# Kernel tuning notes

Hardware: AMD Instinct MI355X
Metric: run time of the kernel (lower is better)

Reference implementation:

```python
import jax, jax.numpy as jnp
import numpy as np

EPS = 1e-5
NUM_HEADS = 8

def _bn(x, w, b, m, v):
    # inference-mode BatchNorm2d over channel dim of (B,C,H,W)
    inv = w / jnp.sqrt(v + EPS)
    return x * inv[None, :, None, None] + (b - m * inv)[None, :, None, None]

def _conv1x1(x, W, b):
    # 1x1 conv == per-pixel matmul: W is (out_ch, in_ch)
    return jnp.einsum('bchw,ec->behw', x, W) + b[None, :, None, None]

def _forward(x, bn1_w, bn1_b, bn1_m, bn1_v, Wq, bq, Wk, bk, Wv, bv, gamma, temperature,
             conv_w, conv_b, cbn_w, cbn_b, cbn_m, cbn_v, rs_w, rs_b, rbn_w, rbn_b, rbn_m, rbn_v):
    B, C, Wd, Hd = x.shape
    S = Wd * Hd
    E = Wq.shape[0]
    hd = E // NUM_HEADS
    xa = jax.nn.relu(_bn(x, bn1_w, bn1_b, bn1_m, bn1_v))
    def proj(Wm, bm):
        return _conv1x1(xa, Wm, bm).reshape(B, NUM_HEADS, hd, S).transpose(0, 1, 3, 2)  # (B,h,S,d)
    q = proj(Wq, bq)
    k = proj(Wk, bk)
    v = proj(Wv, bv)
    scores = jnp.einsum('bhsd,bhtd->bhst', q, k) / temperature  # (B,h,S,S)
    scores = scores - jnp.max(scores, axis=-1, keepdims=True)   # redundant amax-subtract as in source
    attn = jax.nn.softmax(scores, axis=-1)
    out = jnp.einsum('bhst,bhtd->bhsd', attn, v)
    out = out.transpose(0, 1, 3, 2).reshape(B, E, Wd, Hd)
    conv_path = jax.nn.relu(_bn(_conv1x1(x, conv_w, conv_b), cbn_w, cbn_b, cbn_m, cbn_v))
    fused = gamma[0] * out + conv_path
    return jax.nn.gelu(_bn(_conv1x1(fused, rs_w, rs_b), rbn_w, rbn_b, rbn_m, rbn_v), approximate=False)

def setup_inputs() -> dict:
    key = jax.random.key(0)
    ks = jax.random.split(key, 18)
    C, E = 256, 512
    n = lambda k, s, sc=0.02: jax.random.normal(k, s, jnp.float32) * sc
    return {
        'x': jax.random.normal(ks[0], (1, C, 64, 64), jnp.float32),
        'bn1_w': 1.0 + n(ks[1], (C,), 0.1), 'bn1_b': n(ks[2], (C,), 0.1),
        'bn1_m': n(ks[3], (C,), 0.05), 'bn1_v': 0.5 + jax.random.uniform(ks[4], (C,), jnp.float32),
        'Wq': n(ks[5], (E, C)), 'bq': jnp.zeros((E,), jnp.float32),
        'Wk': n(ks[6], (E, C)), 'bk': jnp.zeros((E,), jnp.float32),
        'Wv': n(ks[7], (E, C)), 'bv': jnp.zeros((E,), jnp.float32),
        'gamma': jnp.full((1,), 0.5, jnp.float32),
        'temperature': jnp.asarray(0.85, jnp.float32),
        'conv_w': n(ks[8], (E, C)), 'conv_b': jnp.zeros((E,), jnp.float32),
        'cbn_w': 1.0 + n(ks[9], (E,), 0.1), 'cbn_b': n(ks[10], (E,), 0.1),
        'cbn_m': n(ks[11], (E,), 0.05), 'cbn_v': 0.5 + jax.random.uniform(ks[12], (E,), jnp.float32),
        'rs_w': n(ks[13], (C, E)), 'rs_b': jnp.zeros((C,), jnp.float32),
        'rbn_w': 1.0 + n(ks[14], (C,), 0.1), 'rbn_b': n(ks[15], (C,), 0.1),
        'rbn_m': n(ks[16], (C,), 0.05), 'rbn_v': 0.5 + jax.random.uniform(ks[17], (C,), jnp.float32),
    }

def reference(x, bn1_w, bn1_b, bn1_m, bn1_v, Wq, bq, Wk, bk, Wv, bv, gamma, temperature,
              conv_w, conv_b, cbn_w, cbn_b, cbn_m, cbn_v, rs_w, rs_b, rbn_w, rbn_b, rbn_m, rbn_v):
    return _forward(x, bn1_w, bn1_b, bn1_m, bn1_v, Wq, bq, Wk, bk, Wv, bv, gamma, temperature,
                    conv_w, conv_b, cbn_w, cbn_b, cbn_m, cbn_v, rs_w, rs_b, rbn_w, rbn_b, rbn_m, rbn_v)
```

## Files before the change

kernel.cpp:

```cpp
#include <hip/hip_runtime.h>

#define S_DIM 4096
#define C_IN  256
#define E_DIM 512
#define HD    64
#define EPSV  1e-5f

typedef __attribute__((ext_vector_type(8))) short s8v;
typedef __attribute__((ext_vector_type(4))) short s4v;
typedef __attribute__((ext_vector_type(4))) float f4v;
typedef __attribute__((ext_vector_type(16))) float f16v;

__device__ __forceinline__ float bf2f(unsigned short h){
  union{unsigned u; float f;} v; v.u = ((unsigned)h)<<16; return v.f;
}
__device__ __forceinline__ unsigned short f2bf(float f){
  union{float f; unsigned u;} v; v.f = f;
  unsigned r = v.u + 0x7fffu + ((v.u>>16)&1u);
  return (unsigned short)(r>>16);
}
__device__ __forceinline__ unsigned cvtpk_bf16(float lo, float hi_){
  unsigned r;
  asm("v_cvt_pk_bf16_f32 %0, %1, %2" : "=v"(r) : "v"(lo), "v"(hi_));
  return r;
}
__device__ __forceinline__ s8v lds_rd8(const unsigned short* b, int row, int ck){
  return *(const s8v*)&b[(row<<6) + (((ck)^(row&7))<<3)];
}
__device__ __forceinline__ void lds_wr8(unsigned short* b, int row, int ck, s8v v){
  *(s8v*)&b[(row<<6) + (((ck)^(row&7))<<3)] = v;
}
__device__ __forceinline__ s4v lds_rd4q(const unsigned short* b, int row, int q4){
  return *(const s4v*)&b[(row<<6) + (((q4)^(row&15))<<2)];
}
__device__ __forceinline__ void gl_lds16(const unsigned short* g, unsigned short* l){
  __builtin_amdgcn_global_load_lds(
      (const __attribute__((address_space(1))) unsigned int*)g,
      (__attribute__((address_space(3))) unsigned int*)l, 16, 0, 0);
}

__global__ __launch_bounds__(256) void k_wcvt(const float* __restrict__ w0,
    const float* __restrict__ w1, const float* __restrict__ w2,
    const float* __restrict__ w3, const float* __restrict__ w4,
    unsigned short* __restrict__ dst){
  int i = blockIdx.x*256 + threadIdx.x;
  int z = blockIdx.y;
  const float* s = (z==0)?w0:(z==1)?w1:(z==2)?w2:(z==3)?w3:w4;
  dst[z*(E_DIM*C_IN) + i] = f2bf(s[i]);
}

__global__ __launch_bounds__(256) void k_prep(const float* __restrict__ x,
    const float* __restrict__ bw, const float* __restrict__ bb,
    const float* __restrict__ bm, const float* __restrict__ bvar,
    unsigned short* __restrict__ XaT, unsigned short* __restrict__ XrT){
  __shared__ float tile[32][33];
  int tid = threadIdx.x;
  int tx = tid & 31, ty = tid >> 5;
  int s0 = blockIdx.x*32, c0 = blockIdx.y*32;
  #pragma unroll
  for(int p=0;p<4;p++){
    int c = c0 + ty + p*8;
    tile[ty+p*8][tx] = x[c*S_DIM + s0 + tx];
  }
  __syncthreads();
  int cc = c0 + tx;
  float inv  = bw[cc] * rsqrtf(bvar[cc] + EPSV);
  float beta = bb[cc] - bm[cc]*inv;
  #pragma unroll
  for(int p=0;p<4;p++){
    int s = s0 + ty + p*8;
    float v = tile[tx][ty+p*8];
    float a = v*inv + beta; a = a>0.f?a:0.f;
    XaT[s*C_IN + cc] = f2bf(a);
    XrT[s*C_IN + cc] = f2bf(v);
  }
}

__global__ __launch_bounds__(256) void k_proj(
    const unsigned short* __restrict__ XaT, const unsigned short* __restrict__ XrT,
    const unsigned short* __restrict__ Wb,
    const float* __restrict__ bq, const float* __restrict__ bk,
    const float* __restrict__ bvb, const float* __restrict__ bc,
    const float* __restrict__ cw, const float* __restrict__ cbb,
    const float* __restrict__ cm, const float* __restrict__ cvv,
    unsigned short* __restrict__ QT, unsigned short* __restrict__ KT,
    unsigned short* __restrict__ Vx, unsigned short* __restrict__ CT){
  int z = blockIdx.z;
  const unsigned short* Xin = (z==3) ? XrT : XaT;
  const unsigned short* W   = Wb + z*(E_DIM*C_IN);
  const float* bias = (z==0)?bq:(z==1)?bk:(z==2)?bvb:bc;

  __shared__ unsigned short Als[128*64];
  __shared__ unsigned short Bls[64*64];
  int tid = threadIdx.x;
  int w = tid>>6, l = tid&63, g = l>>4, c16 = l&15;
  int wr = w>>1, wc = w&1;
  int s0 = blockIdx.x*128, e0 = blockIdx.y*64;

  f4v acc[4][2];
  #pragma unroll
  for(int m=0;m<4;m++)
    #pragma unroll
    for(int n=0;n<2;n++) acc[m][n] = (f4v){0.f,0.f,0.f,0.f};

  for(int kk=0;kk<4;kk++){
    __syncthreads();
    #pragma unroll
    for(int p=0;p<4;p++){
      int ck = p*256 + tid, row = ck>>3, ch = ck&7;
      s8v v = *(const s8v*)&Xin[(s0+row)*C_IN + kk*64 + ch*8];
      lds_wr8(Als, row, ch, v);
    }
    #pragma unroll
    for(int p=0;p<2;p++){
      int ck = p*256 + tid, row = ck>>3, ch = ck&7;
      s8v v = *(const s8v*)&W[(e0+row)*C_IN + kk*64 + ch*8];
      lds_wr8(Bls, row, ch, v);
    }
    __syncthreads();
    #pragma unroll
    for(int kb=0;kb<2;kb++){
      s8v bfr[2];
      #pragma unroll
      for(int n=0;n<2;n++) bfr[n] = lds_rd8(Bls, wc*32 + n*16 + c16, g + kb*4);
      #pragma unroll
      for(int m=0;m<4;m++){
        s8v af = lds_rd8(Als, wr*64 + m*16 + c16, g + kb*4);
        #pragma unroll
        for(int n=0;n<2;n++)
          acc[m][n] = __builtin_amdgcn_mfma_f32_16x16x32_bf16(af, bfr[n], acc[m][n], 0,0,0);
      }
    }
  }
  #pragma unroll
  for(int n=0;n<2;n++){
    int e = e0 + wc*32 + n*16 + c16;
    float bsv = bias[e];
    float cinv = 0.f, cbeta = 0.f;
    if(z==3){ cinv = cw[e]*rsqrtf(cvv[e]+EPSV); cbeta = cbb[e] - cm[e]*cinv; }
    #pragma unroll
    for(int m=0;m<4;m++){
      int sb = s0 + wr*64 + m*16 + g*4;
      if(z==2){
        s4v pk;
        #pragma unroll
        for(int i=0;i<4;i++) pk[i] = (short)f2bf(acc[m][n][i] + bsv);
        int sb2 = (sb & ~63) | ((((sb>>2)&15) ^ (e&15))<<2);
        *(s4v*)&Vx[e*S_DIM + sb2] = pk;
      } else {
        unsigned short* dst = (z==0)?QT:(z==1)?KT:CT;
        #pragma unroll
        for(int i=0;i<4;i++){
          float vv = acc[m][n][i] + bsv;
          if(z==3){ vv = vv*cinv + cbeta; vv = vv>0.f?vv:0.f; }
          int key = sb+i;
          int ee = e;
          if(z==1) ee = (e & ~56) | ((((e>>3)&7) ^ (key&7))<<3);
          dst[key*E_DIM + ee] = f2bf(vv);
        }
      }
    }
  }
}

__global__ __launch_bounds__(512,2) void k_attn(
    const unsigned short* __restrict__ QT, const unsigned short* __restrict__ KT,
    const unsigned short* __restrict__ Vx, const unsigned short* __restrict__ CT,
    const float* __restrict__ gamma, const float* __restrict__ temp,
    unsigned short* __restrict__ fusedT){
  __shared__ unsigned short SM[65536];
  int tid = threadIdx.x;
  int w = tid>>6, l = tid&63, l31 = l&31, hi = l>>5;
  int qh = w>>2, kh = w&3;
  int bx = blockIdx.x;
  int h = bx&7;
  int q0b = (bx>>3)*128;
  float scl = 1.4426950408889634f / temp[0];

  #define STAGE_K(BUF, T) { \
    _Pragma("unroll") \
    for(int j=0;j<4;j++){ \
      int c = w*4 + j; int flat = c*64 + l; \
      int tile = flat>>9, gg = flat&511, row = gg>>3, ch = gg&7; \
      int sK = tile*1024 + (T)*64; \
      gl_lds16(&KT[(sK+row)*E_DIM + h*HD + ch*8], SM + (BUF)*32768 + c*512); \
    } }
  #define STAGE_V(BUF, T) { \
    _Pragma("unroll") \
    for(int j=0;j<4;j++){ \
      int c = 32 + w*4 + j; int flat = c*64 + l; \
      int tile = (flat>>9)&3, gg = flat&511, row = gg>>3, ch = gg&7; \
      int sK = tile*1024 + (T)*64; \
      gl_lds16(&Vx[(h*HD+row)*S_DIM + sK + ch*8], SM + (BUF)*32768 + c*512); \
    } }

  STAGE_K(0, 0);
  STAGE_V(0, 0);

  s8v qf[2][4];
  #pragma unroll
  for(int qg=0;qg<2;qg++){
    int q = q0b + qh*64 + qg*32 + l31;
    #pragma unroll
    for(int ks=0;ks<4;ks++){
      s8v r = *(const s8v*)&QT[q*E_DIM + h*HD + ks*16 + hi*8];
      #pragma unroll
      for(int j=0;j<8;j++) qf[qg][ks][j] = (short)f2bf(bf2f((unsigned short)r[j])*scl);
    }
  }

  f16v oacc[2][2];
  #pragma unroll
  for(int qg=0;qg<2;qg++)
    #pragma unroll
    for(int dt=0;dt<2;dt++)
      #pragma unroll
      for(int r=0;r<16;r++) oacc[qg][dt][r]=0.f;
  float lrun[2] = {0.f, 0.f};

  int buf = 0;
  #pragma unroll 1
  for(int t=0;t<16;t++){
    asm volatile("s_waitcnt vmcnt(4)" ::: "memory");
    __builtin_amdgcn_s_barrier();
    if(t<15) STAGE_K(buf^1, t+1);
    const unsigned short* Kb = SM + buf*32768 + kh*4096;

    union{ s8v v; unsigned u[4]; } pa[2][2][2];
    #pragma unroll
    for(int sub=0;sub<2;sub++){
      int kr = sub*32 + l31;
      s8v kf[4];
      #pragma unroll
      for(int ks=0;ks<4;ks++) kf[ks] = lds_rd8(Kb, kr, ks*2 + hi);
      #pragma unroll
      for(int qg=0;qg<2;qg++){
        f16v d;
        #pragma unroll
        for(int r=0;r<16;r++) d[r]=0.f;
        __builtin_amdgcn_s_setprio(1);
        #pragma unroll
        for(int ks=0;ks<4;ks++)
          d = __builtin_amdgcn_mfma_f32_32x32x16_bf16(kf[ks], qf[qg][ks], d, 0,0,0);
        __builtin_amdgcn_s_setprio(0);
        float e_[16], ls = 0.f;
        #pragma unroll
        for(int r=0;r<16;r++){ e_[r] = __builtin_amdgcn_exp2f(d[r]); ls += e_[r]; }
        lrun[qg] += ls;
        #pragma unroll
        for(int j=0;j<4;j++){
          pa[sub][qg][0].u[j] = cvtpk_bf16(e_[2*j],   e_[2*j+1]);
          pa[sub][qg][1].u[j] = cvtpk_bf16(e_[8+2*j], e_[8+2*j+1]);
        }
      }
    }

    if(t<15){ asm volatile("s_waitcnt vmcnt(4)" ::: "memory"); }
    else    { asm volatile("s_waitcnt vmcnt(0)" ::: "memory"); }
    __builtin_amdgcn_s_barrier();
    if(t<15) STAGE_V(buf^1, t+1);
    const unsigned short* Vb = SM + buf*32768 + (4+kh)*4096;

    __builtin_amdgcn_s_setprio(1);
    #pragma unroll
    for(int sub=0;sub<2;sub++){
      #pragma unroll
      for(int dt=0;dt<2;dt++){
        int vr = dt*32 + l31;
        union{ s8v v; s4v h2[2]; } vf;
        vf.h2[0] = lds_rd4q(Vb, vr, sub*8 + hi);
        vf.h2[1] = lds_rd4q(Vb, vr, sub*8 + 2 + hi);
        oacc[0][dt] = __builtin_amdgcn_mfma_f32_32x32x16_bf16(pa[sub][0][0].v, vf.v, oacc[0][dt], 0,0,0);
        oacc[1][dt] = __builtin_amdgcn_mfma_f32_32x32x16_bf16(pa[sub][1][0].v, vf.v, oacc[1][dt], 0,0,0);
        vf.h2[0] = lds_rd4q(Vb, vr, sub*8 + 4 + hi);
        vf.h2[1] = lds_rd4q(Vb, vr, sub*8 + 6 + hi);
        oacc[0][dt] = __builtin_amdgcn_mfma_f32_32x32x16_bf16(pa[sub][0][1].v, vf.v, oacc[0][dt], 0,0,0);
        oacc[1][dt] = __builtin_amdgcn_mfma_f32_32x32x16_bf16(pa[sub][1][1].v, vf.v, oacc[1][dt], 0,0,0);
      }
    }
    __builtin_amdgcn_s_setprio(0);
    buf ^= 1;
  }

  #pragma unroll
  for(int qg=0;qg<2;qg++) lrun[qg] += __shfl_xor(lrun[qg], 32);

  float* slab = (float*)SM;
  float* l_buf = slab + 6*64*33;
  float ga = gamma[0];
  #pragma unroll
  for(int qg=0;qg<2;qg++){
    __syncthreads();
    if(kh!=0){
      float* dst = slab + ((qh*3 + (kh-1))*64 + l)*33;
      #pragma unroll
      for(int r=0;r<16;r++){ dst[r] = oacc[qg][0][r]; dst[16+r] = oacc[qg][1][r]; }
      dst[32] = lrun[qg];
    }
    __syncthreads();
    float lt = 0.f;
    if(kh==0){
      lt = lrun[qg];
      #pragma unroll
      for(int s=0;s<3;s++){
        const float* src = slab + ((qh*3 + s)*64 + l)*33;
        #pragma unroll
        for(int r=0;r<16;r++){ oacc[qg][0][r] += src[r]; oacc[qg][1][r] += src[16+r]; }
        lt += src[32];
      }
      if(hi==0) l_buf[qh*32 + l31] = lt;
    }
    __syncthreads();
    if(kh==0){
      #pragma unroll
      for(int dt=0;dt<2;dt++){
        int e = h*HD + dt*32 + l31;
        #pragma unroll
        for(int g4=0;g4<4;g4++){
          float4 lv = *(float4*)&l_buf[qh*32 + g4*8 + hi*4];
          float la[4] = {lv.x, lv.y, lv.z, lv.w};
          #pragma unroll
          for(int j=0;j<4;j++){
            int r = g4*4 + j;
            int qrow = q0b + qh*64 + qg*32 + j + g4*8 + hi*4;
            float o = oacc[qg][dt][r]*(ga/la[j]) + bf2f(CT[qrow*E_DIM + e]);
            fusedT[qrow*E_DIM + e] = f2bf(o);
          }
        }
      }
    }
  }
  #undef STAGE_K
  #undef STAGE_V
}

__global__ __launch_bounds__(256) void k_final(
    const unsigned short* __restrict__ Wrs,
    const unsigned short* __restrict__ fusedT,
    const float* __restrict__ rsb,
    const float* __restrict__ rw, const float* __restrict__ rbb,
    const float* __restrict__ rm, const float* __restrict__ rv,
    float* __restrict__ out){
  __shared__ unsigned short Als[64*64];
  __shared__ unsigned short Bls[64*64];
  int tid = threadIdx.x;
  int w = tid>>6, l = tid&63, g = l>>4, c16 = l&15;
  int wr2 = w>>1, wc2 = w&1;
  int sB0 = blockIdx.x*64, c0 = blockIdx.y*64;
  f4v acc[2][2];
  #pragma unroll
  for(int m=0;m<2;m++)
    #pragma unroll
    for(int n=0;n<2;n++) acc[m][n]=(f4v){0.f,0.f,0.f,0.f};
  for(int kk=0;kk<8;kk++){
    __syncthreads();
    #pragma unroll
    for(int p=0;p<2;p++){
      int ck = p*256+tid, row=ck>>3, ch=ck&7;
      s8v v = *(const s8v*)&Wrs[(c0+row)*E_DIM + kk*64 + ch*8];
      lds_wr8(Als, row, ch, v);
    }
    #pragma unroll
    for(int p=0;p<2;p++){
      int ck = p*256+tid, row=ck>>3, ch=ck&7;
      s8v v = *(const s8v*)&fusedT[(sB0+row)*E_DIM + kk*64 + ch*8];
      lds_wr8(Bls, row, ch, v);
    }
    __syncthreads();
    #pragma unroll
    for(int kb=0;kb<2;kb++){
      s8v af[2]; s8v bfr[2];
      #pragma unroll
      for(int m=0;m<2;m++) af[m] = lds_rd8(Als, wr2*32 + m*16 + c16, g + kb*4);
      #pragma unroll
      for(int n=0;n<2;n++) bfr[n] = lds_rd8(Bls, wc2*32 + n*16 + c16, g + kb*4);
      #pragma unroll
      for(int m=0;m<2;m++)
        #pragma unroll
        for(int n=0;n<2;n++)
          acc[m][n] = __builtin_amdgcn_mfma_f32_16x16x32_bf16(af[m], bfr[n], acc[m][n],0,0,0);
    }
  }
  #pragma unroll
  for(int m=0;m<2;m++){
    #pragma unroll
    for(int i=0;i<4;i++){
      int c = c0 + wr2*32 + m*16 + g*4 + i;
      float bias = rsb[c];
      float rinv = rw[c]*rsqrtf(rv[c]+EPSV);
      float rbeta = rbb[c] - rm[c]*rinv;
      #pragma unroll
      for(int n=0;n<2;n++){
        int s = sB0 + wc2*32 + n*16 + c16;
        float vv = acc[m][n][i] + bias;
        vv = vv*rinv + rbeta;
        out[c*S_DIM + s] = 0.5f*vv*(1.0f + erff(vv*0.70710678118f));
      }
    }
  }
}

extern "C" void kernel_launch(void* const* d_in, const int* in_sizes, int n_in,
                              void* d_out, int out_size, void* d_ws, size_t ws_size,
                              hipStream_t stream){
  const float* x     = (const float*)d_in[0];
  const float* bn1w  = (const float*)d_in[1];
  const float* bn1b  = (const float*)d_in[2];
  const float* bn1m  = (const float*)d_in[3];
  const float* bn1v  = (const float*)d_in[4];
  const float* Wq    = (const float*)d_in[5];
  const float* bq    = (const float*)d_in[6];
  const float* Wk    = (const float*)d_in[7];
  const float* bk    = (const float*)d_in[8];
  const float* Wv    = (const float*)d_in[9];
  const float* bv    = (const float*)d_in[10];
  const float* gamma = (const float*)d_in[11];
  const float* temp  = (const float*)d_in[12];
  const float* convw = (const float*)d_in[13];
  const float* convb = (const float*)d_in[14];
  const float* cbnw  = (const float*)d_in[15];
  const float* cbnb  = (const float*)d_in[16];
  const float* cbnm  = (const float*)d_in[17];
  const float* cbnv  = (const float*)d_in[18];
  const float* rsw   = (const float*)d_in[19];
  const float* rsbp  = (const float*)d_in[20];
  const float* rbnw  = (const float*)d_in[21];
  const float* rbnb  = (const float*)d_in[22];
  const float* rbnm  = (const float*)d_in[23];
  const float* rbnv  = (const float*)d_in[24];
  float* out = (float*)d_out;

  unsigned short* ws  = (unsigned short*)d_ws;
  unsigned short* XaT = ws;
  unsigned short* XrT = XaT + S_DIM*C_IN;
  unsigned short* Wb  = XrT + S_DIM*C_IN;
  unsigned short* Wrs = Wb + 4*E_DIM*C_IN;
  unsigned short* QT  = Wrs + C_IN*E_DIM;
  unsigned short* KT  = QT + S_DIM*E_DIM;
  unsigned short* Vx  = KT + S_DIM*E_DIM;
  unsigned short* CT  = Vx + S_DIM*E_DIM;
  unsigned short* fusedT = CT + S_DIM*E_DIM;

  k_wcvt<<<dim3(512,5),256,0,stream>>>(Wq, Wk, Wv, convw, rsw, Wb);
  k_prep<<<dim3(128,8),256,0,stream>>>(x, bn1w, bn1b, bn1m, bn1v, XaT, XrT);
  k_proj<<<dim3(32,8,4),256,0,stream>>>(XaT, XrT, Wb, bq, bk, bv, convb,
                                        cbnw, cbnb, cbnm, cbnv, QT, KT, Vx, CT);
  k_attn<<<dim3(256),512,0,stream>>>(QT, KT, Vx, CT, gamma, temp, fusedT);
  k_final<<<dim3(64,4),256,0,stream>>>(Wrs, fusedT, rsbp, rbnw, rbnb, rbnm, rbnv, out);
}
```

Baseline: 88.89 us.

## Split attention into smaller 256-thread blocks with 32-key tiles

Attention blocks shrink from 512 threads covering 128 queries to 256 threads covering 64 queries, doubling the grid to 512 blocks. Key/value tiles per step drop from 64 to 32 keys, so there are twice as many iterations. K and V are staged together in one step with a single wait per iteration, and the V layout swizzle in the projection kernel is changed to match. The aim is better occupancy and load balance across CUs with less LDS per block, at the cost of each K/V tile being reused by fewer queries and more barriers.

```diff
diff --git a/kernel.cpp b/kernel.cpp
--- a/kernel.cpp
+++ b/kernel.cpp
@@ -30,8 +30,8 @@
 __device__ __forceinline__ void lds_wr8(unsigned short* b, int row, int ck, s8v v){
   *(s8v*)&b[(row<<6) + (((ck)^(row&7))<<3)] = v;
 }
-__device__ __forceinline__ s4v lds_rd4q(const unsigned short* b, int row, int q4){
-  return *(const s4v*)&b[(row<<6) + (((q4)^(row&15))<<2)];
+__device__ __forceinline__ s4v lds_rd4v(const unsigned short* b, int row, int q4){
+  return *(const s4v*)&b[(row<<5) + (((q4) ^ ((row>>1)&7))<<2)];
 }
 __device__ __forceinline__ void gl_lds16(const unsigned short* g, unsigned short* l){
   __builtin_amdgcn_global_load_lds(
@@ -145,7 +145,7 @@
         s4v pk;
         #pragma unroll
         for(int i=0;i<4;i++) pk[i] = (short)f2bf(acc[m][n][i] + bsv);
-        int sb2 = (sb & ~63) | ((((sb>>2)&15) ^ (e&15))<<2);
+        int sb2 = (sb & ~31) | ((((sb>>2)&7) ^ ((e>>1)&7))<<2);
         *(s4v*)&Vx[e*S_DIM + sb2] = pk;
       } else {
         unsigned short* dst = (z==0)?QT:(z==1)?KT:CT;
@@ -163,44 +163,37 @@
   }
 }
 
-__global__ __launch_bounds__(512,2) void k_attn(
+__global__ __launch_bounds__(256,2) void k_attn(
     const unsigned short* __restrict__ QT, const unsigned short* __restrict__ KT,
     const unsigned short* __restrict__ Vx, const unsigned short* __restrict__ CT,
     const float* __restrict__ gamma, const float* __restrict__ temp,
     unsigned short* __restrict__ fusedT){
-  __shared__ unsigned short SM[65536];
+  __shared__ unsigned short SM[32768];
   int tid = threadIdx.x;
-  int w = tid>>6, l = tid&63, l31 = l&31, hi = l>>5;
-  int qh = w>>2, kh = w&3;
+  int kh = tid>>6, l = tid&63, l31 = l&31, hi = l>>5;
   int bx = blockIdx.x;
   int h = bx&7;
-  int q0b = (bx>>3)*128;
+  int q0b = (bx>>3)*64;
   float scl = 1.4426950408889634f / temp[0];
 
-  #define STAGE_K(BUF, T) { \
+  #define STAGE(B, T) { \
+    int sK = kh*1024 + (T)*32; \
     _Pragma("unroll") \
-    for(int j=0;j<4;j++){ \
-      int c = w*4 + j; int flat = c*64 + l; \
-      int tile = flat>>9, gg = flat&511, row = gg>>3, ch = gg&7; \
-      int sK = tile*1024 + (T)*64; \
-      gl_lds16(&KT[(sK+row)*E_DIM + h*HD + ch*8], SM + (BUF)*32768 + c*512); \
-    } }
-  #define STAGE_V(BUF, T) { \
+    for(int j=0;j<4;j++) \
+      gl_lds16(&KT[(sK + j*8 + (l>>3))*E_DIM + h*HD + (l&7)*8], \
+               SM + (B)*16384 + kh*2048 + j*512); \
     _Pragma("unroll") \
-    for(int j=0;j<4;j++){ \
-      int c = 32 + w*4 + j; int flat = c*64 + l; \
-      int tile = (flat>>9)&3, gg = flat&511, row = gg>>3, ch = gg&7; \
-      int sK = tile*1024 + (T)*64; \
-      gl_lds16(&Vx[(h*HD+row)*S_DIM + sK + ch*8], SM + (BUF)*32768 + c*512); \
-    } }
-
-  STAGE_K(0, 0);
-  STAGE_V(0, 0);
+    for(int j=0;j<4;j++) \
+      gl_lds16(&Vx[(h*HD + j*16 + (l>>2))*S_DIM + sK + (l&3)*8], \
+               SM + (B)*16384 + 8192 + kh*2048 + j*512); \
+  }
+
+  STAGE(0, 0);
 
   s8v qf[2][4];
   #pragma unroll
   for(int qg=0;qg<2;qg++){
-    int q = q0b + qh*64 + qg*32 + l31;
+    int q = q0b + qg*32 + l31;
     #pragma unroll
     for(int ks=0;ks<4;ks++){
       s8v r = *(const s8v*)&QT[q*E_DIM + h*HD + ks*16 + hi*8];
@@ -220,65 +213,62 @@
 
   int buf = 0;
   #pragma unroll 1
-  for(int t=0;t<16;t++){
-    asm volatile("s_waitcnt vmcnt(4)" ::: "memory");
+  for(int t=0;t<32;t++){
+    if(t<31){
+      STAGE(buf^1, t+1);
+      asm volatile("s_waitcnt vmcnt(8)" ::: "memory");
+    } else {
+      asm volatile("s_waitcnt vmcnt(0)" ::: "memory");
+    }
     __builtin_amdgcn_s_barrier();
-    if(t<15) STAGE_K(buf^1, t+1);
-    const unsigned short* Kb = SM + buf*32768 + kh*4096;
-
-    union{ s8v v; unsigned u[4]; } pa[2][2][2];
-    #pragma unroll
-    for(int sub=0;sub<2;sub++){
-      int kr = sub*32 + l31;
-      s8v kf[4];
-      #pragma unroll
-      for(int ks=0;ks<4;ks++) kf[ks] = lds_rd8(Kb, kr, ks*2 + hi);
-      #pragma unroll
-      for(int qg=0;qg<2;qg++){
-        f16v d;
-        #pragma unroll
-        for(int r=0;r<16;r++) d[r]=0.f;
-        __builtin_amdgcn_s_setprio(1);
-        #pragma unroll
-        for(int ks=0;ks<4;ks++)
-          d = __builtin_amdgcn_mfma_f32_32x32x16_bf16(kf[ks], qf[qg][ks], d, 0,0,0);
-        __builtin_amdgcn_s_setprio(0);
-        float e_[16], ls = 0.f;
-        #pragma unroll
-        for(int r=0;r<16;r++){ e_[r] = __builtin_amdgcn_exp2f(d[r]); ls += e_[r]; }
-        lrun[qg] += ls;
-        #pragma unroll
-        for(int j=0;j<4;j++){
-          pa[sub][qg][0].u[j] = cvtpk_bf16(e_[2*j],   e_[2*j+1]);
-          pa[sub][qg][1].u[j] = cvtpk_bf16(e_[8+2*j], e_[8+2*j+1]);
-        }
-      }
-    }
-
-    if(t<15){ asm volatile("s_waitcnt vmcnt(4)" ::: "memory"); }
-    else    { asm volatile("s_waitcnt vmcnt(0)" ::: "memory"); }
+
+    const unsigned short* Kb = SM + buf*16384 + kh*2048;
+    const unsigned short* Vb = SM + buf*16384 + 8192 + kh*2048;
+
+    s8v kf[4];
+    #pragma unroll
+    for(int ks=0;ks<4;ks++) kf[ks] = lds_rd8(Kb, l31, ks*2 + hi);
+
+    union{ s8v v; unsigned u[4]; } pa[2][2];
+    #pragma unroll
+    for(int qg=0;qg<2;qg++){
+      f16v d;
+      #pragma unroll
+      for(int r=0;r<16;r++) d[r]=0.f;
+      __builtin_amdgcn_s_setprio(1);
+      #pragma unroll
+      for(int ks=0;ks<4;ks++)
+        d = __builtin_amdgcn_mfma_f32_32x32x16_bf16(kf[ks], qf[qg][ks], d, 0,0,0);
+      __builtin_amdgcn_s_setprio(0);
+      float e_[16], ls = 0.f;
+      #pragma unroll
+      for(int r=0;r<16;r++){ e_[r] = __builtin_amdgcn_exp2f(d[r]); ls += e_[r]; }
+      lrun[qg] += ls;
+      #pragma unroll
+      for(int j=0;j<4;j++){
+        pa[qg][0].u[j] = cvtpk_bf16(e_[2*j],   e_[2*j+1]);
+        pa[qg][1].u[j] = cvtpk_bf16(e_[8+2*j], e_[8+2*j+1]);
+      }
+    }
+
+    __builtin_amdgcn_s_setprio(1);
+    #pragma unroll
+    for(int dt=0;dt<2;dt++){
+      int vr = dt*32 + l31;
+      union{ s8v v; s4v h2[2]; } vf;
+      vf.h2[0] = lds_rd4v(Vb, vr, hi);
+      vf.h2[1] = lds_rd4v(Vb, vr, 2 + hi);
+      oacc[0][dt] = __builtin_amdgcn_mfma_f32_32x32x16_bf16(pa[0][0].v, vf.v, oacc[0][dt], 0,0,0);
+      oacc[1][dt] = __builtin_amdgcn_mfma_f32_32x32x16_bf16(pa[1][0].v, vf.v, oacc[1][dt], 0,0,0);
+      vf.h2[0] = lds_rd4v(Vb, vr, 4 + hi);
+      vf.h2[1] = lds_rd4v(Vb, vr, 6 + hi);
+      oacc[0][dt] = __builtin_amdgcn_mfma_f32_32x32x16_bf16(pa[0][1].v, vf.v, oacc[0][dt], 0,0,0);
+      oacc[1][dt] = __builtin_amdgcn_mfma_f32_32x32x16_bf16(pa[1][1].v, vf.v, oacc[1][dt], 0,0,0);
+    }
+    __builtin_amdgcn_s_setprio(0);
+
+    __builtin_amdgcn_sched_barrier(0);
     __builtin_amdgcn_s_barrier();
-    if(t<15) STAGE_V(buf^1, t+1);
-    const unsigned short* Vb = SM + buf*32768 + (4+kh)*4096;
-
-    __builtin_amdgcn_s_setprio(1);
-    #pragma unroll
-    for(int sub=0;sub<2;sub++){
-      #pragma unroll
-      for(int dt=0;dt<2;dt++){
-        int vr = dt*32 + l31;
-        union{ s8v v; s4v h2[2]; } vf;
-        vf.h2[0] = lds_rd4q(Vb, vr, sub*8 + hi);
-        vf.h2[1] = lds_rd4q(Vb, vr, sub*8 + 2 + hi);
-        oacc[0][dt] = __builtin_amdgcn_mfma_f32_32x32x16_bf16(pa[sub][0][0].v, vf.v, oacc[0][dt], 0,0,0);
-        oacc[1][dt] = __builtin_amdgcn_mfma_f32_32x32x16_bf16(pa[sub][1][0].v, vf.v, oacc[1][dt], 0,0,0);
-        vf.h2[0] = lds_rd4q(Vb, vr, sub*8 + 4 + hi);
-        vf.h2[1] = lds_rd4q(Vb, vr, sub*8 + 6 + hi);
-        oacc[0][dt] = __builtin_amdgcn_mfma_f32_32x32x16_bf16(pa[sub][0][1].v, vf.v, oacc[0][dt], 0,0,0);
-        oacc[1][dt] = __builtin_amdgcn_mfma_f32_32x32x16_bf16(pa[sub][1][1].v, vf.v, oacc[1][dt], 0,0,0);
-      }
-    }
-    __builtin_amdgcn_s_setprio(0);
     buf ^= 1;
   }
 
@@ -286,43 +276,39 @@
   for(int qg=0;qg<2;qg++) lrun[qg] += __shfl_xor(lrun[qg], 32);
 
   float* slab = (float*)SM;
-  float* l_buf = slab + 6*64*33;
+  float* l_buf = slab + 3*64*33;
   float ga = gamma[0];
   #pragma unroll
   for(int qg=0;qg<2;qg++){
     __syncthreads();
     if(kh!=0){
-      float* dst = slab + ((qh*3 + (kh-1))*64 + l)*33;
+      float* dst = slab + (((kh-1))*64 + l)*33;
       #pragma unroll
       for(int r=0;r<16;r++){ dst[r] = oacc[qg][0][r]; dst[16+r] = oacc[qg][1][r]; }
       dst[32] = lrun[qg];
     }
     __syncthreads();
-    float lt = 0.f;
     if(kh==0){
-      lt = lrun[qg];
+      float lt = lrun[qg];
       #pragma unroll
       for(int s=0;s<3;s++){
-        const float* src = slab + ((qh*3 + s)*64 + l)*33;
+        const float* src = slab + ((s)*64 + l)*33;
         #pragma unroll
         for(int r=0;r<16;r++){ oacc[qg][0][r] += src[r]; oacc[qg][1][r] += src[16+r]; }
         lt += src[32];
       }
-      if(hi==0) l_buf[qh*32 + l31] = lt;
-    }
-    __syncthreads();
-    if(kh==0){
+      if(hi==0) l_buf[l31] = lt;
       #pragma unroll
       for(int dt=0;dt<2;dt++){
         int e = h*HD + dt*32 + l31;
         #pragma unroll
         for(int g4=0;g4<4;g4++){
-          float4 lv = *(float4*)&l_buf[qh*32 + g4*8 + hi*4];
+          float4 lv = *(float4*)&l_buf[g4*8 + hi*4];
           float la[4] = {lv.x, lv.y, lv.z, lv.w};
           #pragma unroll
           for(int j=0;j<4;j++){
             int r = g4*4 + j;
-            int qrow = q0b + qh*64 + qg*32 + j + g4*8 + hi*4;
+            int qrow = q0b + qg*32 + j + g4*8 + hi*4;
             float o = oacc[qg][dt][r]*(ga/la[j]) + bf2f(CT[qrow*E_DIM + e]);
             fusedT[qrow*E_DIM + e] = f2bf(o);
           }
@@ -330,8 +316,7 @@
       }
     }
   }
-  #undef STAGE_K
-  #undef STAGE_V
+  #undef STAGE
 }
 
 __global__ __launch_bounds__(256) void k_final(
@@ -445,6 +430,6 @@
   k_prep<<<dim3(128,8),256,0,stream>>>(x, bn1w, bn1b, bn1m, bn1v, XaT, XrT);
   k_proj<<<dim3(32,8,4),256,0,stream>>>(XaT, XrT, Wb, bq, bk, bv, convb,
                                         cbnw, cbnb, cbnm, cbnv, QT, KT, Vx, CT);
-  k_attn<<<dim3(256),512,0,stream>>>(QT, KT, Vx, CT, gamma, temp, fusedT);
+  k_attn<<<dim3(512),256,0,stream>>>(QT, KT, Vx, CT, gamma, temp, fusedT);
   k_final<<<dim3(64,4),256,0,stream>>>(Wrs, fusedT, rsbp, rbnw, rbnb, rbnm, rbnv, out);
 }
```

Result: slower. 93.71 us (+5.4%).
